# Kernel tuning notes

Measured on AMD Instinct MI355X. Metric: run time of the kernel, lower is better.

Reference implementation:

```python
import jax, jax.numpy as jnp
import numpy as np

B, T, E = 2, 2048, 2048
H, KV, D = 16, 4, 128
N_REP = H // KV
WINDOW = 512
BASE_THETA = 10000.0
MIN_VAL = -1e9


def _rope_cos_sin(seq_len, dim, dtype):
    inv_freq = 1.0 / (BASE_THETA ** (jnp.arange(0, dim, 2, dtype=jnp.float32) / dim))
    ang = jnp.arange(seq_len, dtype=jnp.float32)[:, None] * inv_freq[None, :]  # [T, D/2]
    return jnp.cos(ang).astype(dtype), jnp.sin(ang).astype(dtype)


def _apply_rope(x, cos, sin):
    # x: [B, T, h, D]; rotate-half convention
    x1, x2 = jnp.split(x, 2, axis=-1)
    c = cos[None, :, None, :]
    s = sin[None, :, None, :]
    return jnp.concatenate([x1 * c - x2 * s, x2 * c + x1 * s], axis=-1)


def setup_inputs() -> dict:
    key = jax.random.key(0)
    k1, k2, k3, k4, k5 = jax.random.split(key, 5)
    std = 0.02 / np.sqrt(2 * 24)
    return {
        "x": jax.random.normal(k1, (B, T, E), dtype=jnp.float32),
        "Wq": jax.random.normal(k2, (H * D, E), dtype=jnp.float32) * std,
        "Wk": jax.random.normal(k3, (KV * D, E), dtype=jnp.float32) * std,
        "Wv": jax.random.normal(k4, (KV * D, E), dtype=jnp.float32) * std,
        "Wo": jax.random.normal(k5, (E, E), dtype=jnp.float32) * std,
    }


def reference(x, Wq, Wk, Wv, Wo):
    b, t, e = x.shape
    scale = 1.0 / jnp.sqrt(jnp.float32(D))

    q = (x @ Wq.T).reshape(b, t, H, D)
    k = (x @ Wk.T).reshape(b, t, KV, D)
    v = (x @ Wv.T).reshape(b, t, KV, D)

    cos, sin = _rope_cos_sin(t, D, x.dtype)
    q = _apply_rope(q, cos, sin)
    k = _apply_rope(k, cos, sin)

    # GQA: repeat kv heads to match query heads
    k = jnp.repeat(k, N_REP, axis=2)  # [B, T, H, D]
    v = jnp.repeat(v, N_REP, axis=2)

    scores = jnp.einsum("bqhd,bkhd->bhqk", q, k) * scale  # [B, H, T, T]

    # sliding-window causal additive mask (offset=0)
    rows = jnp.arange(t)[:, None]
    cols = jnp.arange(t)[None, :]
    valid = (cols <= rows) & ((rows - cols) < WINDOW)
    mask = jnp.where(valid, 0.0, MIN_VAL).astype(x.dtype)  # [T, T]
    scores = scores + mask[None, None, :, :]

    attn = jax.nn.softmax(scores, axis=-1)
    out = jnp.einsum("bhqk,bkhd->bqhd", attn, v).reshape(b, t, H * D)
    return out @ Wo.T
```

## Files before the change

### kernel.cpp

```cpp
#include <hip/hip_runtime.h>
#include <hip/hip_bf16.h>
#include <cstdint>

#define TSEQ 2048
#define NB   2
#define NH   16
#define NKV  4
#define HD   128
#define EMB  2048
#define WIN  512

typedef unsigned short u16;
typedef __attribute__((ext_vector_type(8))) short s16x8;
typedef __attribute__((ext_vector_type(4))) float f32x4;
typedef __attribute__((ext_vector_type(16))) float f32x16;
typedef __attribute__((ext_vector_type(4))) unsigned short u16x4;
typedef __attribute__((ext_vector_type(8))) unsigned short u16x8;

__device__ __forceinline__ u16 f2bf(float x) {
    unsigned u = __builtin_bit_cast(unsigned, x);
    u += 0x7fffu + ((u >> 16) & 1u);
    return (u16)(u >> 16);
}
__device__ __forceinline__ float bf2f(u16 u) {
    return __builtin_bit_cast(float, ((unsigned)u) << 16);
}
__device__ __forceinline__ float ex2(float x) {
    return __builtin_amdgcn_exp2f(x);
}

__device__ __forceinline__ void gld_lds16(const void* g, void* l) {
    __builtin_amdgcn_global_load_lds(
        (__attribute__((address_space(1))) void*)(void*)(g),
        (__attribute__((address_space(3))) void*)(l),
        16, 0, 0);
}

__device__ __forceinline__ f32x4 mfma16(s16x8 a, s16x8 b, f32x4 c) {
    return __builtin_amdgcn_mfma_f32_16x16x32_bf16(a, b, c, 0, 0, 0);
}
__device__ __forceinline__ f32x16 mfma32(s16x8 a, s16x8 b, f32x16 c) {
    return __builtin_amdgcn_mfma_f32_32x32x16_bf16(a, b, c, 0, 0, 0);
}

template <int CTRL>
__device__ __forceinline__ float dpp_movf(float x) {
    return __builtin_bit_cast(float,
        __builtin_amdgcn_update_dpp(0, __builtin_bit_cast(int, x), CTRL, 0xF, 0xF, true));
}
__device__ __forceinline__ float dpp_max16(float x) {
    x = fmaxf(x, dpp_movf<0xB1>(x));
    x = fmaxf(x, dpp_movf<0x4E>(x));
    x = fmaxf(x, dpp_movf<0x128>(x));
    x = fmaxf(x, dpp_movf<0x124>(x));
    return x;
}
__device__ __forceinline__ float dpp_sum16(float x) {
    x += dpp_movf<0xB1>(x);
    x += dpp_movf<0x4E>(x);
    x += dpp_movf<0x128>(x);
    x += dpp_movf<0x124>(x);
    return x;
}

__global__ void cast_all(const float* __restrict__ x,  const float* __restrict__ wq,
                         const float* __restrict__ wk, const float* __restrict__ wv,
                         const float* __restrict__ wo,
                         u16* __restrict__ xb, u16* __restrict__ wqb,
                         u16* __restrict__ wkvb, u16* __restrict__ wob,
                         float* __restrict__ tab) {
    if (blockIdx.x >= 18432) {
        int i = (blockIdx.x - 18432) * 256 + threadIdx.x;
        int t = i >> 6, d = i & 63;
        float inv = __expf(-(float)d * (9.210340371976184f / 64.0f));
        float s, c;
        sincosf((float)t * inv, &s, &c);
        tab[i] = c;
        tab[131072 + i] = s;
        return;
    }
    long i = ((long)blockIdx.x * 256 + threadIdx.x) * 4;
    const float* s; u16* d; long off;
    if (i < 8388608L)        { s = x;  d = xb;             off = i; }
    else if (i < 12582912L)  { s = wq; d = wqb;            off = i - 8388608L; }
    else if (i < 13631488L)  { s = wk; d = wkvb;           off = i - 12582912L; }
    else if (i < 14680064L)  { s = wv; d = wkvb + 1048576; off = i - 13631488L; }
    else                     { s = wo; d = wob;            off = i - 14680064L; }
    float4 v = *(const float4*)(s + off);
    u16x4 o;
    o[0] = f2bf(v.x); o[1] = f2bf(v.y); o[2] = f2bf(v.z); o[3] = f2bf(v.w);
    *(u16x4*)(d + off) = o;
}

template <int MODE>
__global__ __launch_bounds__(256) void gemm_bt(const u16* __restrict__ A, const u16* __restrict__ B,
                                               void* __restrict__ Cp, u16* __restrict__ vtp,
                                               u16* __restrict__ kp,
                                               int M, int N, int K) {
    __shared__ __align__(16) u16 smem[16384];
    u16* As = smem;
    u16* Bs = smem + 8192;
    const int tid  = threadIdx.x;
    const int lane = tid & 63;
    const int w    = tid >> 6;
    const int l31  = lane & 31;
    const int half = lane >> 5;
    const int wr   = w >> 1, wc = w & 1;

    const int srow   = w * 8 + (lane >> 3);
    const int schunk = lane & 7;
    const u16* agp[4];
    const u16* bgp[4];
#pragma unroll
    for (int s = 0; s < 4; s++) {
        const int row = s * 32 + srow;
        const int sig = ((row >> 1) ^ (row >> 2)) & 7;
        agp[s] = A + (size_t)(blockIdx.y * 128 + row) * K + (schunk ^ sig) * 8;
        bgp[s] = B + (size_t)(blockIdx.x * 128 + row) * K + (schunk ^ sig) * 8;
    }

    int sigA[2], sigB[2];
#pragma unroll
    for (int i = 0; i < 2; i++) {
        const int ra = wr * 64 + i * 32 + l31;
        sigA[i] = ((ra >> 1) ^ (ra >> 2)) & 7;
        const int rb = wc * 64 + i * 32 + l31;
        sigB[i] = ((rb >> 1) ^ (rb >> 2)) & 7;
    }

    f32x16 acc[2][2];
#pragma unroll
    for (int i = 0; i < 2; i++)
#pragma unroll
        for (int j = 0; j < 2; j++)
#pragma unroll
            for (int r = 0; r < 16; r++)
                acc[i][j][r] = 0.f;

    for (int k0 = 0; k0 < K; k0 += 64) {
#pragma unroll
        for (int s = 0; s < 4; s++) {
            gld_lds16(agp[s], (char*)As + (s * 32 + w * 8) * 128);
            agp[s] += 64;
        }
#pragma unroll
        for (int s = 0; s < 4; s++) {
            gld_lds16(bgp[s], (char*)Bs + (s * 32 + w * 8) * 128);
            bgp[s] += 64;
        }
        __syncthreads();
        s16x8 af[2][4], bf[2][4];
#pragma unroll
        for (int i = 0; i < 2; i++)
#pragma unroll
            for (int ks = 0; ks < 4; ks++)
                af[i][ks] = *(const s16x8*)((char*)As + (wr * 64 + i * 32 + l31) * 128 +
                                            ((half + ks * 2) ^ sigA[i]) * 16);
#pragma unroll
        for (int j = 0; j < 2; j++)
#pragma unroll
            for (int ks = 0; ks < 4; ks++)
                bf[j][ks] = *(const s16x8*)((char*)Bs + (wc * 64 + j * 32 + l31) * 128 +
                                            ((half + ks * 2) ^ sigB[j]) * 16);
#pragma unroll
        for (int ks = 0; ks < 4; ks++)
#pragma unroll
            for (int i = 0; i < 2; i++)
#pragma unroll
                for (int j = 0; j < 2; j++)
                    acc[i][j] = mfma32(af[i][ks], bf[j][ks], acc[i][j]);
        __syncthreads();
    }

    const int row0 = blockIdx.y * 128 + wr * 64;
    const int col0 = blockIdx.x * 128 + wc * 64 + l31;

    if (MODE == 0) {
#pragma unroll
        for (int i = 0; i < 2; i++)
#pragma unroll
            for (int j = 0; j < 2; j++)
#pragma unroll
                for (int r = 0; r < 16; r++) {
                    const int crow = row0 + i * 32 + (r & 3) + 8 * (r >> 2) + 4 * half;
                    ((float*)Cp)[(size_t)crow * N + col0 + j * 32] = acc[i][j][r];
                }
    } else {
        if (blockIdx.x < 16) {
#pragma unroll
            for (int i = 0; i < 2; i++)
#pragma unroll
                for (int j = 0; j < 2; j++)
#pragma unroll
                    for (int r = 0; r < 16; r++) {
                        const int crow = row0 + i * 32 + (r & 3) + 8 * (r >> 2) + 4 * half;
                        ((u16*)Cp)[(size_t)crow * 2048 + col0 + j * 32] = f2bf(acc[i][j][r]);
                    }
        } else if (blockIdx.x < 20) {
            const int kcol0 = col0 - 2048;
#pragma unroll
            for (int i = 0; i < 2; i++)
#pragma unroll
                for (int j = 0; j < 2; j++)
#pragma unroll
                    for (int r = 0; r < 16; r++) {
                        const int crow = row0 + i * 32 + (r & 3) + 8 * (r >> 2) + 4 * half;
                        kp[(size_t)crow * 512 + kcol0 + j * 32] = f2bf(acc[i][j][r]);
                    }
        } else {
            const int kvi = blockIdx.x - 20;
            const int bb  = (blockIdx.y * 128) >> 11;
            const int tl0 = (blockIdx.y * 128) & (TSEQ - 1);
            u16* tr = smem;
#pragma unroll
            for (int p = 0; p < 2; p++) {
                __syncthreads();
                if (wc == p) {
#pragma unroll
                    for (int i = 0; i < 2; i++)
#pragma unroll
                        for (int j = 0; j < 2; j++)
#pragma unroll
                            for (int r = 0; r < 16; r++) {
                                const int tl = wr * 64 + i * 32 + (r & 3) + 8 * (r >> 2) + 4 * half;
                                tr[(j * 32 + l31) * 136 + tl] = f2bf(acc[i][j][r]);
                            }
                }
                __syncthreads();
#pragma unroll
                for (int s = 0; s < 4; s++) {
                    int slot = s * 256 + tid;
                    int dr = slot >> 4;
                    int tc = slot & 15;
                    u16x8 val = *(const u16x8*)(tr + dr * 136 + tc * 8);
                    *(u16x8*)(vtp + ((size_t)((bb * NKV + kvi) * HD + p * 64 + dr)) * TSEQ +
                              tl0 + tc * 8) = val;
                }
            }
        }
    }
}

__global__ void rope_k(u16* __restrict__ buf, const float* __restrict__ tab) {
    int i = blockIdx.x * 256 + threadIdx.x;
    int d   = i & 63;
    int hh  = (i >> 6) & 3;
    int row = i >> 8;
    int t   = row & (TSEQ - 1);
    size_t base = (size_t)row * 512 + hh * HD + d;
    float x1 = bf2f(buf[base]);
    float x2 = bf2f(buf[base + 64]);
    float c = tab[t * 64 + d];
    float s = tab[131072 + t * 64 + d];
    buf[base]      = f2bf(x1 * c - x2 * s);
    buf[base + 64] = f2bf(x2 * c + x1 * s);
}

__global__ __launch_bounds__(256, 3) void attn_kernel(const u16* __restrict__ qb, const u16* __restrict__ kb,
                                                      const u16* __restrict__ vt, const float* __restrict__ tab,
                                                      u16* __restrict__ ao) {
    __shared__ __align__(16) char smem[40960];
    u16* ks = (u16*)smem;
    u16* vs = (u16*)(smem + 16384);
    u16* Pl = (u16*)(smem + 32768);

    const int tid  = threadIdx.x;
    const int w    = tid >> 6;
    const int lane = tid & 63;
    const int l15  = lane & 15;
    const int quad = lane >> 4;
    const int id   = blockIdx.x;
    const int kv   = id & 3;
    const int b    = (id >> 2) & 1;
    const int q0   = (id >> 3) * 16;
    const int h    = kv * 4 + w;
    u16* Pw = Pl + w * 1024;
    const float scale2 = 0.1275174089593282f;

    const u16* kbase = kb + (size_t)b * TSEQ * 512 + kv * HD;
    const u16* vbase = vt + (size_t)(b * NKV + kv) * HD * TSEQ;

    s16x8 aq[4];
    {
        const u16* qrow = qb + (size_t)(b * TSEQ + q0 + l15) * EMB + h * HD + quad * 8;
        const float* ct = tab + (size_t)(q0 + l15) * 64 + quad * 8;
        float qf[4][8], cs[2][8], sn[2][8];
        *(float4*)(&cs[0][0]) = *(const float4*)(ct);
        *(float4*)(&cs[0][4]) = *(const float4*)(ct + 4);
        *(float4*)(&cs[1][0]) = *(const float4*)(ct + 32);
        *(float4*)(&cs[1][4]) = *(const float4*)(ct + 36);
        *(float4*)(&sn[0][0]) = *(const float4*)(ct + 131072);
        *(float4*)(&sn[0][4]) = *(const float4*)(ct + 131076);
        *(float4*)(&sn[1][0]) = *(const float4*)(ct + 131104);
        *(float4*)(&sn[1][4]) = *(const float4*)(ct + 131108);
#pragma unroll
        for (int c = 0; c < 4; c++)
#pragma unroll
            for (int e = 0; e < 8; e++)
                qf[c][e] = bf2f(qrow[c * 32 + e]);
#pragma unroll
        for (int c = 0; c < 2; c++)
#pragma unroll
            for (int e = 0; e < 8; e++) {
                float x1 = qf[c][e], x2 = qf[c + 2][e];
                qf[c][e]     = x1 * cs[c][e] - x2 * sn[c][e];
                qf[c + 2][e] = x2 * cs[c][e] + x1 * sn[c][e];
            }
#pragma unroll
        for (int c = 0; c < 4; c++)
#pragma unroll
            for (int e = 0; e < 8; e++)
                aq[c][e] = (short)f2bf(qf[c][e]);
    }

    f32x4 o[8];
#pragma unroll
    for (int n = 0; n < 8; n++) o[n] = f32x4{0.f, 0.f, 0.f, 0.f};
    float mrow[4] = {-1e30f, -1e30f, -1e30f, -1e30f};
    float lrow[4] = {0.f, 0.f, 0.f, 0.f};

    int kb0 = q0 - (WIN - 1);
    if (kb0 < 0) kb0 = 0;
    kb0 &= ~63;

    for (int kbi = kb0; kbi <= q0 + 15; kbi += 64) {
#pragma unroll
        for (int s = 0; s < 4; s++) {
            int slot = s * 256 + tid;
            int i    = slot >> 4;
            int lc   = (slot & 15) ^ (i & 7);
            gld_lds16(kbase + (size_t)(kbi + i) * 512 + lc * 8, (char*)ks + slot * 16);
        }
#pragma unroll
        for (int s = 0; s < 4; s++) {
            int slot = s * 256 + tid;
            int d    = slot >> 3;
            int lc   = (slot & 7) ^ (d & 7);
            gld_lds16(vbase + (size_t)d * TSEQ + kbi + lc * 8, (char*)vs + slot * 16);
        }
        __syncthreads();

        f32x4 sv[4];
#pragma unroll
        for (int kt = 0; kt < 4; kt++) sv[kt] = f32x4{0.f, 0.f, 0.f, 0.f};
#pragma unroll
        for (int c = 0; c < 4; c++) {
            s16x8 bk[4];
#pragma unroll
            for (int kt = 0; kt < 4; kt++) {
                int sc = (c * 4 + quad) ^ (l15 & 7);
                bk[kt] = *(const s16x8*)(ks + (kt * 16 + l15) * 128 + sc * 8);
            }
#pragma unroll
            for (int kt = 0; kt < 4; kt++)
                sv[kt] = mfma16(aq[c], bk[kt], sv[kt]);
        }

        const bool full = (kbi >= q0 - 496) && (kbi + 63 <= q0);
        float alpha[4], p[4][4];
#pragma unroll
        for (int r = 0; r < 4; r++) {
            const int row = q0 + quad * 4 + r;
            float v[4];
            if (full) {
#pragma unroll
                for (int kt = 0; kt < 4; kt++) v[kt] = sv[kt][r] * scale2;
            } else {
#pragma unroll
                for (int kt = 0; kt < 4; kt++) {
                    int cidx = kbi + kt * 16 + l15;
                    v[kt] = (cidx <= row && row - cidx < WIN) ? sv[kt][r] * scale2 : -1e30f;
                }
            }
            float mx = fmaxf(fmaxf(v[0], v[1]), fmaxf(v[2], v[3]));
            mx = dpp_max16(mx);
            float mnew = fmaxf(mrow[r], mx);
            alpha[r] = ex2(mrow[r] - mnew);
            float e0 = ex2(v[0] - mnew);
            float e1 = ex2(v[1] - mnew);
            float e2 = ex2(v[2] - mnew);
            float e3 = ex2(v[3] - mnew);
            float rs = (e0 + e1) + (e2 + e3);
            rs = dpp_sum16(rs);
            lrow[r] = lrow[r] * alpha[r] + rs;
            mrow[r] = mnew;
            p[0][r] = e0; p[1][r] = e1; p[2][r] = e2; p[3][r] = e3;
        }
#pragma unroll
        for (int n = 0; n < 8; n++) {
            o[n][0] *= alpha[0]; o[n][1] *= alpha[1];
            o[n][2] *= alpha[2]; o[n][3] *= alpha[3];
        }

#pragma unroll
        for (int r = 0; r < 4; r++)
#pragma unroll
            for (int kt = 0; kt < 4; kt++)
                Pw[(kt >> 1) * 512 + (quad * 4 + r) * 32 + (kt & 1) * 16 + l15] = f2bf(p[kt][r]);
        asm volatile("s_waitcnt lgkmcnt(0)" ::: "memory");
        s16x8 ap0 = *(const s16x8*)(Pw + l15 * 32 + quad * 8);
        s16x8 ap1 = *(const s16x8*)(Pw + 512 + l15 * 32 + quad * 8);

#pragma unroll
        for (int n = 0; n < 8; n++) {
            int sc = quad ^ (l15 & 7);
            s16x8 bv = *(const s16x8*)(vs + (n * 16 + l15) * 64 + sc * 8);
            o[n] = mfma16(ap0, bv, o[n]);
        }
#pragma unroll
        for (int n = 0; n < 8; n++) {
            int sc = (4 + quad) ^ (l15 & 7);
            s16x8 bv = *(const s16x8*)(vs + (n * 16 + l15) * 64 + sc * 8);
            o[n] = mfma16(ap1, bv, o[n]);
        }
        __syncthreads();
    }

    float linv[4];
#pragma unroll
    for (int r = 0; r < 4; r++) linv[r] = 1.0f / lrow[r];
    u16* Ow = (u16*)(smem + w * 4352);
#pragma unroll
    for (int n = 0; n < 8; n++)
#pragma unroll
        for (int r = 0; r < 4; r++)
            Ow[(quad * 4 + r) * 136 + n * 16 + l15] = f2bf(o[n][r] * linv[r]);
    asm volatile("s_waitcnt lgkmcnt(0)" ::: "memory");
#pragma unroll
    for (int s = 0; s < 4; s++) {
        int row = s * 4 + quad;
        u16x8 val = *(const u16x8*)(Ow + row * 136 + l15 * 8);
        *(u16x8*)(ao + (size_t)(b * TSEQ + q0 + row) * EMB + h * HD + l15 * 8) = val;
    }
}

extern "C" void kernel_launch(void* const* d_in, const int* in_sizes, int n_in,
                              void* d_out, int out_size, void* d_ws, size_t ws_size,
                              hipStream_t stream) {
    const float* x  = (const float*)d_in[0];
    const float* Wq = (const float*)d_in[1];
    const float* Wk = (const float*)d_in[2];
    const float* Wv = (const float*)d_in[3];
    const float* Wo = (const float*)d_in[4];
    float* out = (float*)d_out;

    u16* ws   = (u16*)d_ws;
    u16* xb   = ws;
    u16* wqb  = ws + 8388608L;
    u16* wkvb = ws + 12582912L;
    u16* wob  = ws + 14680064L;
    u16* qb   = ws + 18874368L;
    u16* kbuf = ws + 27262976L;
    u16* vt   = ws + 29360128L;
    float* tab = (float*)(ws + 31457280L);
    u16* ao   = xb;

    cast_all<<<18944, 256, 0, stream>>>(x, Wq, Wk, Wv, Wo, xb, wqb, wkvb, wob, tab);

    gemm_bt<3><<<dim3(24, 32), 256, 0, stream>>>(xb, wqb, qb, vt, kbuf, 4096, 3072, 2048);

    rope_k<<<4096, 256, 0, stream>>>(kbuf, tab);

    attn_kernel<<<1024, 256, 0, stream>>>(qb, kbuf, vt, tab, ao);

    gemm_bt<0><<<dim3(16, 32), 256, 0, stream>>>(ao, wob, out, nullptr, nullptr, 4096, 2048, 2048);
}
```

Measured before the change: 255.1 us.

## Rewrite GEMMs as 8-wave double-buffered kernels with larger tiles and interleaved loads

Replaces the 256-thread 128x128 GEMM with a 512-thread kernel using 256x256 tiles for the QKV projection and 256x128 tiles for the output projection. LDS is double-buffered, and global-to-LDS loads for tile t+2 are issued between MFMA phases, with partial vmcnt waits, barriers and s_setprio to overlap memory with compute. The aim is more operand reuse and hidden load latency in both projection GEMMs. The cost is fewer blocks (192 and 256) on a 256-CU part, plus higher register and LDS pressure.

```diff
diff --git a/kernel.cpp b/kernel.cpp
--- a/kernel.cpp
+++ b/kernel.cpp
@@ -92,149 +92,259 @@
     *(u16x4*)(d + off) = o;
 }
 
+#define RDFRAG(base, offb, sg, ks) \
+    (*(const s16x8*)((base) + (offb) + ((((half) + 2 * (ks)) ^ (sg)) << 4)))
+
 template <int MODE>
-__global__ __launch_bounds__(256) void gemm_bt(const u16* __restrict__ A, const u16* __restrict__ B,
-                                               void* __restrict__ Cp, u16* __restrict__ vtp,
-                                               u16* __restrict__ kp,
-                                               int M, int N, int K) {
-    __shared__ __align__(16) u16 smem[16384];
-    u16* As = smem;
-    u16* Bs = smem + 8192;
+__global__ __launch_bounds__(512) void gemm8(const u16* __restrict__ A, const u16* __restrict__ B,
+                                             void* __restrict__ Cp, u16* __restrict__ vtp,
+                                             u16* __restrict__ kp) {
+    constexpr int BN     = (MODE == 3) ? 256 : 128;
+    constexpr int NBB    = BN / 64;
+    constexpr int MT     = (MODE == 3) ? 4 : 2;
+    constexpr int WM     = MT * 32;
+    constexpr int K      = 2048;
+    constexpr int NTK    = K / 64;
+    constexpr int ABYTES = 32768;
+    constexpr int BBYTES = BN * 128;
+    constexpr int BUFB   = ABYTES + BBYTES;
+
+    __shared__ __align__(16) char smem[2 * BUFB];
+
     const int tid  = threadIdx.x;
     const int lane = tid & 63;
     const int w    = tid >> 6;
     const int l31  = lane & 31;
     const int half = lane >> 5;
-    const int wr   = w >> 1, wc = w & 1;
+    const int wr   = (MODE == 3) ? (w >> 2) : (w >> 1);
+    const int wc   = (MODE == 3) ? (w & 3) : (w & 1);
+    const int bx   = blockIdx.x, by = blockIdx.y;
 
     const int srow   = w * 8 + (lane >> 3);
     const int schunk = lane & 7;
+    const int sdoff  = w * 8 * 128;
+
     const u16* agp[4];
-    const u16* bgp[4];
+    const u16* bgp[NBB];
 #pragma unroll
     for (int s = 0; s < 4; s++) {
-        const int row = s * 32 + srow;
-        const int sig = ((row >> 1) ^ (row >> 2)) & 7;
-        agp[s] = A + (size_t)(blockIdx.y * 128 + row) * K + (schunk ^ sig) * 8;
-        bgp[s] = B + (size_t)(blockIdx.x * 128 + row) * K + (schunk ^ sig) * 8;
-    }
-
-    int sigA[2], sigB[2];
-#pragma unroll
-    for (int i = 0; i < 2; i++) {
-        const int ra = wr * 64 + i * 32 + l31;
-        sigA[i] = ((ra >> 1) ^ (ra >> 2)) & 7;
-        const int rb = wc * 64 + i * 32 + l31;
-        sigB[i] = ((rb >> 1) ^ (rb >> 2)) & 7;
-    }
-
-    f32x16 acc[2][2];
-#pragma unroll
-    for (int i = 0; i < 2; i++)
-#pragma unroll
-        for (int j = 0; j < 2; j++)
+        const int row = s * 64 + srow;
+        const int sg  = ((row >> 1) ^ (row >> 2)) & 7;
+        agp[s] = A + (size_t)(by * 256 + row) * K + ((schunk ^ sg) << 3);
+    }
+#pragma unroll
+    for (int s = 0; s < NBB; s++) {
+        const int row = s * 64 + srow;
+        const int sg  = ((row >> 1) ^ (row >> 2)) & 7;
+        bgp[s] = B + (size_t)(bx * BN + row) * K + ((schunk ^ sg) << 3);
+    }
+
+    int aoffb[MT], asg[MT];
+#pragma unroll
+    for (int mi = 0; mi < MT; mi++) {
+        const int r = wr * WM + mi * 32 + l31;
+        aoffb[mi] = r * 128;
+        asg[mi]   = ((r >> 1) ^ (r >> 2)) & 7;
+    }
+    int boffb[2], bsg[2];
+#pragma unroll
+    for (int nj = 0; nj < 2; nj++) {
+        const int r = wc * 64 + nj * 32 + l31;
+        boffb[nj] = r * 128;
+        bsg[nj]   = ((r >> 1) ^ (r >> 2)) & 7;
+    }
+
+    f32x16 acc[MT][2];
+#pragma unroll
+    for (int mi = 0; mi < MT; mi++)
+#pragma unroll
+        for (int nj = 0; nj < 2; nj++)
 #pragma unroll
             for (int r = 0; r < 16; r++)
-                acc[i][j][r] = 0.f;
-
-    for (int k0 = 0; k0 < K; k0 += 64) {
-#pragma unroll
-        for (int s = 0; s < 4; s++) {
-            gld_lds16(agp[s], (char*)As + (s * 32 + w * 8) * 128);
-            agp[s] += 64;
-        }
-#pragma unroll
-        for (int s = 0; s < 4; s++) {
-            gld_lds16(bgp[s], (char*)Bs + (s * 32 + w * 8) * 128);
+                acc[mi][nj][r] = 0.f;
+
+    auto stage_a02 = [&](char* base) {
+        gld_lds16(agp[0], base + sdoff);          agp[0] += 64;
+        gld_lds16(agp[2], base + 16384 + sdoff);  agp[2] += 64;
+    };
+    auto stage_rest = [&](char* base) {
+        gld_lds16(agp[1], base + 8192 + sdoff);   agp[1] += 64;
+        gld_lds16(agp[3], base + 24576 + sdoff);  agp[3] += 64;
+#pragma unroll
+        for (int s = 0; s < NBB; s++) {
+            gld_lds16(bgp[s], base + ABYTES + s * 8192 + sdoff);
             bgp[s] += 64;
         }
-        __syncthreads();
-        s16x8 af[2][4], bf[2][4];
-#pragma unroll
-        for (int i = 0; i < 2; i++)
+    };
+
+    stage_a02(smem);        stage_rest(smem);
+    stage_a02(smem + BUFB); stage_rest(smem + BUFB);
+
+    for (int t = 0; t < NTK; ++t) {
+        char* buf = smem + (t & 1) * BUFB;
+        const char* Ab = buf;
+        const char* Bb = buf + ABYTES;
+        if (t < NTK - 1) {
+            if constexpr (MODE == 3) asm volatile("s_waitcnt vmcnt(8)" ::: "memory");
+            else                     asm volatile("s_waitcnt vmcnt(6)" ::: "memory");
+        } else {
+            asm volatile("s_waitcnt vmcnt(0)" ::: "memory");
+        }
+        __builtin_amdgcn_s_barrier();
+
+        if constexpr (MODE == 3) {
+            s16x8 aA[4], aB[4], bA[4], bB[4];
+#pragma unroll
+            for (int ks = 0; ks < 4; ks++) {
+                aA[ks] = RDFRAG(Ab, aoffb[0], asg[0], ks);
+                aB[ks] = RDFRAG(Ab, aoffb[1], asg[1], ks);
+                bA[ks] = RDFRAG(Bb, boffb[0], bsg[0], ks);
+            }
+            __builtin_amdgcn_s_barrier();
+            __builtin_amdgcn_s_setprio(1);
+#pragma unroll
+            for (int ks = 0; ks < 4; ks++) {
+                acc[0][0] = mfma32(aA[ks], bA[ks], acc[0][0]);
+                acc[1][0] = mfma32(aB[ks], bA[ks], acc[1][0]);
+            }
+            __builtin_amdgcn_s_setprio(0);
+            __builtin_amdgcn_s_barrier();
 #pragma unroll
             for (int ks = 0; ks < 4; ks++)
-                af[i][ks] = *(const s16x8*)((char*)As + (wr * 64 + i * 32 + l31) * 128 +
-                                            ((half + ks * 2) ^ sigA[i]) * 16);
-#pragma unroll
-        for (int j = 0; j < 2; j++)
+                bB[ks] = RDFRAG(Bb, boffb[1], bsg[1], ks);
+            __builtin_amdgcn_s_barrier();
+            __builtin_amdgcn_s_setprio(1);
+#pragma unroll
+            for (int ks = 0; ks < 4; ks++) {
+                acc[0][1] = mfma32(aA[ks], bB[ks], acc[0][1]);
+                acc[1][1] = mfma32(aB[ks], bB[ks], acc[1][1]);
+            }
+            __builtin_amdgcn_s_setprio(0);
+            __builtin_amdgcn_s_barrier();
+            asm volatile("" ::: "memory");
+            if (t + 2 < NTK) stage_a02(buf);
+#pragma unroll
+            for (int ks = 0; ks < 4; ks++) {
+                aA[ks] = RDFRAG(Ab, aoffb[2], asg[2], ks);
+                aB[ks] = RDFRAG(Ab, aoffb[3], asg[3], ks);
+            }
+            __builtin_amdgcn_s_barrier();
+            __builtin_amdgcn_s_setprio(1);
+#pragma unroll
+            for (int ks = 0; ks < 4; ks++) {
+                acc[2][1] = mfma32(aA[ks], bB[ks], acc[2][1]);
+                acc[3][1] = mfma32(aB[ks], bB[ks], acc[3][1]);
+            }
+            __builtin_amdgcn_s_setprio(0);
+            __builtin_amdgcn_s_barrier();
+            __builtin_amdgcn_s_setprio(1);
+#pragma unroll
+            for (int ks = 0; ks < 4; ks++) {
+                acc[2][0] = mfma32(aA[ks], bA[ks], acc[2][0]);
+                acc[3][0] = mfma32(aB[ks], bA[ks], acc[3][0]);
+            }
+            __builtin_amdgcn_s_setprio(0);
+            __builtin_amdgcn_s_barrier();
+            asm volatile("" ::: "memory");
+            if (t + 2 < NTK) stage_rest(buf);
+        } else {
+            s16x8 aA[4], aB[4], bA[4], bB[4];
+#pragma unroll
+            for (int ks = 0; ks < 4; ks++) {
+                aA[ks] = RDFRAG(Ab, aoffb[0], asg[0], ks);
+                bA[ks] = RDFRAG(Bb, boffb[0], bsg[0], ks);
+                bB[ks] = RDFRAG(Bb, boffb[1], bsg[1], ks);
+            }
+            __builtin_amdgcn_s_barrier();
+            __builtin_amdgcn_s_setprio(1);
+#pragma unroll
+            for (int ks = 0; ks < 4; ks++) {
+                acc[0][0] = mfma32(aA[ks], bA[ks], acc[0][0]);
+                acc[0][1] = mfma32(aA[ks], bB[ks], acc[0][1]);
+            }
+            __builtin_amdgcn_s_setprio(0);
+            __builtin_amdgcn_s_barrier();
 #pragma unroll
             for (int ks = 0; ks < 4; ks++)
-                bf[j][ks] = *(const s16x8*)((char*)Bs + (wc * 64 + j * 32 + l31) * 128 +
-                                            ((half + ks * 2) ^ sigB[j]) * 16);
-#pragma unroll
-        for (int ks = 0; ks < 4; ks++)
-#pragma unroll
-            for (int i = 0; i < 2; i++)
-#pragma unroll
-                for (int j = 0; j < 2; j++)
-                    acc[i][j] = mfma32(af[i][ks], bf[j][ks], acc[i][j]);
-        __syncthreads();
-    }
-
-    const int row0 = blockIdx.y * 128 + wr * 64;
-    const int col0 = blockIdx.x * 128 + wc * 64 + l31;
-
-    if (MODE == 0) {
-#pragma unroll
-        for (int i = 0; i < 2; i++)
-#pragma unroll
-            for (int j = 0; j < 2; j++)
+                aB[ks] = RDFRAG(Ab, aoffb[1], asg[1], ks);
+            __builtin_amdgcn_s_barrier();
+            __builtin_amdgcn_s_setprio(1);
+#pragma unroll
+            for (int ks = 0; ks < 4; ks++) {
+                acc[1][0] = mfma32(aB[ks], bA[ks], acc[1][0]);
+                acc[1][1] = mfma32(aB[ks], bB[ks], acc[1][1]);
+            }
+            __builtin_amdgcn_s_setprio(0);
+            __builtin_amdgcn_s_barrier();
+            asm volatile("" ::: "memory");
+            if (t + 2 < NTK) { stage_a02(buf); stage_rest(buf); }
+        }
+    }
+
+    const int row0 = by * 256 + wr * WM;
+    if constexpr (MODE == 0) {
+        const int col0 = bx * BN + wc * 64 + l31;
+#pragma unroll
+        for (int mi = 0; mi < MT; mi++)
+#pragma unroll
+            for (int nj = 0; nj < 2; nj++)
 #pragma unroll
                 for (int r = 0; r < 16; r++) {
-                    const int crow = row0 + i * 32 + (r & 3) + 8 * (r >> 2) + 4 * half;
-                    ((float*)Cp)[(size_t)crow * N + col0 + j * 32] = acc[i][j][r];
+                    const int crow = row0 + mi * 32 + (r & 3) + 8 * (r >> 2) + 4 * half;
+                    ((float*)Cp)[(size_t)crow * 2048 + col0 + nj * 32] = acc[mi][nj][r];
                 }
     } else {
-        if (blockIdx.x < 16) {
-#pragma unroll
-            for (int i = 0; i < 2; i++)
-#pragma unroll
-                for (int j = 0; j < 2; j++)
+        if (bx < 8) {
+            const int col0 = bx * 256 + wc * 64 + l31;
+#pragma unroll
+            for (int mi = 0; mi < MT; mi++)
+#pragma unroll
+                for (int nj = 0; nj < 2; nj++)
 #pragma unroll
                     for (int r = 0; r < 16; r++) {
-                        const int crow = row0 + i * 32 + (r & 3) + 8 * (r >> 2) + 4 * half;
-                        ((u16*)Cp)[(size_t)crow * 2048 + col0 + j * 32] = f2bf(acc[i][j][r]);
+                        const int crow = row0 + mi * 32 + (r & 3) + 8 * (r >> 2) + 4 * half;
+                        ((u16*)Cp)[(size_t)crow * 2048 + col0 + nj * 32] = f2bf(acc[mi][nj][r]);
                     }
-        } else if (blockIdx.x < 20) {
-            const int kcol0 = col0 - 2048;
-#pragma unroll
-            for (int i = 0; i < 2; i++)
-#pragma unroll
-                for (int j = 0; j < 2; j++)
+        } else if (bx < 10) {
+            const int kcol0 = (bx - 8) * 256 + wc * 64 + l31;
+#pragma unroll
+            for (int mi = 0; mi < MT; mi++)
+#pragma unroll
+                for (int nj = 0; nj < 2; nj++)
 #pragma unroll
                     for (int r = 0; r < 16; r++) {
-                        const int crow = row0 + i * 32 + (r & 3) + 8 * (r >> 2) + 4 * half;
-                        kp[(size_t)crow * 512 + kcol0 + j * 32] = f2bf(acc[i][j][r]);
+                        const int crow = row0 + mi * 32 + (r & 3) + 8 * (r >> 2) + 4 * half;
+                        kp[(size_t)crow * 512 + kcol0 + nj * 32] = f2bf(acc[mi][nj][r]);
                     }
         } else {
-            const int kvi = blockIdx.x - 20;
-            const int bb  = (blockIdx.y * 128) >> 11;
-            const int tl0 = (blockIdx.y * 128) & (TSEQ - 1);
-            u16* tr = smem;
+            const int bb = (by * 256) >> 11;
+            const int t0 = (by * 256) & (TSEQ - 1);
+            u16* tr = (u16*)smem;
 #pragma unroll
             for (int p = 0; p < 2; p++) {
                 __syncthreads();
-                if (wc == p) {
-#pragma unroll
-                    for (int i = 0; i < 2; i++)
-#pragma unroll
-                        for (int j = 0; j < 2; j++)
+                if ((wc >> 1) == p) {
+#pragma unroll
+                    for (int mi = 0; mi < MT; mi++)
+#pragma unroll
+                        for (int nj = 0; nj < 2; nj++)
 #pragma unroll
                             for (int r = 0; r < 16; r++) {
-                                const int tl = wr * 64 + i * 32 + (r & 3) + 8 * (r >> 2) + 4 * half;
-                                tr[(j * 32 + l31) * 136 + tl] = f2bf(acc[i][j][r]);
+                                const int tl = wr * 128 + mi * 32 + (r & 3) + 8 * (r >> 2) + 4 * half;
+                                const int cl = (wc & 1) * 64 + nj * 32 + l31;
+                                tr[cl * 264 + tl] = f2bf(acc[mi][nj][r]);
                             }
                 }
                 __syncthreads();
 #pragma unroll
-                for (int s = 0; s < 4; s++) {
-                    int slot = s * 256 + tid;
-                    int dr = slot >> 4;
-                    int tc = slot & 15;
-                    u16x8 val = *(const u16x8*)(tr + dr * 136 + tc * 8);
-                    *(u16x8*)(vtp + ((size_t)((bb * NKV + kvi) * HD + p * 64 + dr)) * TSEQ +
-                              tl0 + tc * 8) = val;
+                for (int s = 0; s < 8; s++) {
+                    const int slot = s * 512 + tid;
+                    const int dcol = slot >> 5;
+                    const int tseg = slot & 31;
+                    u16x8 val = *(const u16x8*)(tr + dcol * 264 + tseg * 8);
+                    const int vcol = (bx - 10) * 256 + p * 128 + dcol;
+                    *(u16x8*)(vtp + ((size_t)((bb * NKV + (vcol >> 7)) * HD + (vcol & 127))) * TSEQ +
+                              t0 + tseg * 8) = val;
                 }
             }
         }
@@ -457,11 +567,11 @@
 
     cast_all<<<18944, 256, 0, stream>>>(x, Wq, Wk, Wv, Wo, xb, wqb, wkvb, wob, tab);
 
-    gemm_bt<3><<<dim3(24, 32), 256, 0, stream>>>(xb, wqb, qb, vt, kbuf, 4096, 3072, 2048);
+    gemm8<3><<<dim3(12, 16), 512, 0, stream>>>(xb, wqb, qb, vt, kbuf);
 
     rope_k<<<4096, 256, 0, stream>>>(kbuf, tab);
 
     attn_kernel<<<1024, 256, 0, stream>>>(qb, kbuf, vt, tab, ao);
 
-    gemm_bt<0><<<dim3(16, 32), 256, 0, stream>>>(ao, wob, out, nullptr, nullptr, 4096, 2048, 2048);
-}
+    gemm8<0><<<dim3(16, 16), 512, 0, stream>>>(ao, wob, out, nullptr, nullptr);
+}
```

After: 262.2 us. 2.8% more time.

## Double-buffer K/V tiles in attention kernel to overlap loads with compute

Applied to the files above, without the earlier changes.

Attention kernel now keeps two LDS buffers for K and V tiles and issues the async global-to-LDS load for the next key block before computing on the current one. It waits with a partial vmcnt so only the current tile's loads must land. This aims to hide global memory latency behind the MFMA work. In exchange LDS grows to 72KB and the launch-bounds occupancy target drops from 3 to 2 blocks per CU, so there is less latency hiding from extra waves.

```diff
diff --git a/kernel.cpp b/kernel.cpp
--- a/kernel.cpp
+++ b/kernel.cpp
@@ -256,13 +256,13 @@
     buf[base + 64] = f2bf(x2 * c + x1 * s);
 }
 
-__global__ __launch_bounds__(256, 3) void attn_kernel(const u16* __restrict__ qb, const u16* __restrict__ kb,
+__global__ __launch_bounds__(256, 2) void attn_kernel(const u16* __restrict__ qb, const u16* __restrict__ kb,
                                                       const u16* __restrict__ vt, const float* __restrict__ tab,
                                                       u16* __restrict__ ao) {
-    __shared__ __align__(16) char smem[40960];
+    __shared__ __align__(16) char smem[73728];
     u16* ks = (u16*)smem;
-    u16* vs = (u16*)(smem + 16384);
-    u16* Pl = (u16*)(smem + 32768);
+    u16* vs = (u16*)(smem + 32768);
+    u16* Pl = (u16*)(smem + 65536);
 
     const int tid  = threadIdx.x;
     const int w    = tid >> 6;
@@ -322,23 +322,43 @@
     int kb0 = q0 - (WIN - 1);
     if (kb0 < 0) kb0 = 0;
     kb0 &= ~63;
-
-    for (int kbi = kb0; kbi <= q0 + 15; kbi += 64) {
+    const int nt = ((q0 + 15 - kb0) >> 6) + 1;
+
+    auto stage = [&](int kbi, int sel) {
+        char* ksb = (char*)ks + sel * 16384;
+        char* vsb = (char*)vs + sel * 16384;
 #pragma unroll
         for (int s = 0; s < 4; s++) {
             int slot = s * 256 + tid;
             int i    = slot >> 4;
             int lc   = (slot & 15) ^ (i & 7);
-            gld_lds16(kbase + (size_t)(kbi + i) * 512 + lc * 8, (char*)ks + slot * 16);
+            gld_lds16(kbase + (size_t)(kbi + i) * 512 + lc * 8, ksb + slot * 16);
         }
 #pragma unroll
         for (int s = 0; s < 4; s++) {
             int slot = s * 256 + tid;
             int d    = slot >> 3;
             int lc   = (slot & 7) ^ (d & 7);
-            gld_lds16(vbase + (size_t)d * TSEQ + kbi + lc * 8, (char*)vs + slot * 16);
-        }
-        __syncthreads();
+            gld_lds16(vbase + (size_t)d * TSEQ + kbi + lc * 8, vsb + slot * 16);
+        }
+    };
+
+    stage(kb0, 0);
+
+    for (int it = 0; it < nt; ++it) {
+        const int kbi = kb0 + it * 64;
+        const int cur = it & 1;
+        const u16* ksb = (const u16*)((const char*)ks + cur * 16384);
+        const u16* vsb = (const u16*)((const char*)vs + cur * 16384);
+
+        if (it + 1 < nt) {
+            stage(kbi + 64, cur ^ 1);
+            asm volatile("s_waitcnt vmcnt(8)" ::: "memory");
+        } else {
+            asm volatile("s_waitcnt vmcnt(0)" ::: "memory");
+        }
+        __builtin_amdgcn_s_barrier();
+        __builtin_amdgcn_sched_barrier(0);
 
         f32x4 sv[4];
 #pragma unroll
@@ -349,7 +369,7 @@
 #pragma unroll
             for (int kt = 0; kt < 4; kt++) {
                 int sc = (c * 4 + quad) ^ (l15 & 7);
-                bk[kt] = *(const s16x8*)(ks + (kt * 16 + l15) * 128 + sc * 8);
+                bk[kt] = *(const s16x8*)(ksb + (kt * 16 + l15) * 128 + sc * 8);
             }
 #pragma unroll
             for (int kt = 0; kt < 4; kt++)
@@ -404,16 +424,18 @@
 #pragma unroll
         for (int n = 0; n < 8; n++) {
             int sc = quad ^ (l15 & 7);
-            s16x8 bv = *(const s16x8*)(vs + (n * 16 + l15) * 64 + sc * 8);
+            s16x8 bv = *(const s16x8*)(vsb + (n * 16 + l15) * 64 + sc * 8);
             o[n] = mfma16(ap0, bv, o[n]);
         }
 #pragma unroll
         for (int n = 0; n < 8; n++) {
             int sc = (4 + quad) ^ (l15 & 7);
-            s16x8 bv = *(const s16x8*)(vs + (n * 16 + l15) * 64 + sc * 8);
+            s16x8 bv = *(const s16x8*)(vsb + (n * 16 + l15) * 64 + sc * 8);
             o[n] = mfma16(ap1, bv, o[n]);
         }
-        __syncthreads();
+        asm volatile("s_waitcnt lgkmcnt(0)" ::: "memory");
+        __builtin_amdgcn_sched_barrier(0);
+        __builtin_amdgcn_s_barrier();
     }
 
     float linv[4];
```

Result: slower. 266.5 us (+4.5%).

## Fuse K RoPE into QKV GEMM epilogue and raise attention occupancy

Applied to the files above, without the earlier changes.

Applies rotary embedding to K inside the QKV GEMM epilogue by staging the tile in shared memory, which removes the separate rope kernel launch and its global read-modify-write pass. Raises the attention kernel's launch-bounds occupancy hint from 3 to 4 waves per SIMD. Wraps the attention MFMA loops in s_setprio to favour matrix issue. The higher occupancy target may force register spills, and the staged epilogue adds an extra LDS round trip.

```diff
diff --git a/kernel.cpp b/kernel.cpp
--- a/kernel.cpp
+++ b/kernel.cpp
@@ -95,7 +95,7 @@
 template <int MODE>
 __global__ __launch_bounds__(256) void gemm_bt(const u16* __restrict__ A, const u16* __restrict__ B,
                                                void* __restrict__ Cp, u16* __restrict__ vtp,
-                                               u16* __restrict__ kp,
+                                               u16* __restrict__ kp, const float* __restrict__ tab,
                                                int M, int N, int K) {
     __shared__ __align__(16) u16 smem[16384];
     u16* As = smem;
@@ -197,16 +197,33 @@
                         ((u16*)Cp)[(size_t)crow * 2048 + col0 + j * 32] = f2bf(acc[i][j][r]);
                     }
         } else if (blockIdx.x < 20) {
-            const int kcol0 = col0 - 2048;
+            const int head = blockIdx.x - 16;
+            u16* kl = smem;
 #pragma unroll
             for (int i = 0; i < 2; i++)
 #pragma unroll
                 for (int j = 0; j < 2; j++)
 #pragma unroll
                     for (int r = 0; r < 16; r++) {
-                        const int crow = row0 + i * 32 + (r & 3) + 8 * (r >> 2) + 4 * half;
-                        kp[(size_t)crow * 512 + kcol0 + j * 32] = f2bf(acc[i][j][r]);
+                        const int tl = wr * 64 + i * 32 + (r & 3) + 8 * (r >> 2) + 4 * half;
+                        const int cl = wc * 64 + j * 32 + l31;
+                        kl[tl * 128 + cl] = f2bf(acc[i][j][r]);
                     }
+            __syncthreads();
+#pragma unroll
+            for (int s = 0; s < 32; s++) {
+                const int idx = s * 256 + tid;
+                const int row = idx >> 6;
+                const int d   = idx & 63;
+                const float x1 = bf2f(kl[row * 128 + d]);
+                const float x2 = bf2f(kl[row * 128 + d + 64]);
+                const int grow = blockIdx.y * 128 + row;
+                const int t    = grow & (TSEQ - 1);
+                const float c  = tab[t * 64 + d];
+                const float sn = tab[131072 + t * 64 + d];
+                kp[(size_t)grow * 512 + head * 128 + d]      = f2bf(x1 * c - x2 * sn);
+                kp[(size_t)grow * 512 + head * 128 + d + 64] = f2bf(x2 * c + x1 * sn);
+            }
         } else {
             const int kvi = blockIdx.x - 20;
             const int bb  = (blockIdx.y * 128) >> 11;
@@ -241,22 +258,7 @@
     }
 }
 
-__global__ void rope_k(u16* __restrict__ buf, const float* __restrict__ tab) {
-    int i = blockIdx.x * 256 + threadIdx.x;
-    int d   = i & 63;
-    int hh  = (i >> 6) & 3;
-    int row = i >> 8;
-    int t   = row & (TSEQ - 1);
-    size_t base = (size_t)row * 512 + hh * HD + d;
-    float x1 = bf2f(buf[base]);
-    float x2 = bf2f(buf[base + 64]);
-    float c = tab[t * 64 + d];
-    float s = tab[131072 + t * 64 + d];
-    buf[base]      = f2bf(x1 * c - x2 * s);
-    buf[base + 64] = f2bf(x2 * c + x1 * s);
-}
-
-__global__ __launch_bounds__(256, 3) void attn_kernel(const u16* __restrict__ qb, const u16* __restrict__ kb,
+__global__ __launch_bounds__(256, 4) void attn_kernel(const u16* __restrict__ qb, const u16* __restrict__ kb,
                                                       const u16* __restrict__ vt, const float* __restrict__ tab,
                                                       u16* __restrict__ ao) {
     __shared__ __align__(16) char smem[40960];
@@ -343,6 +345,7 @@
         f32x4 sv[4];
 #pragma unroll
         for (int kt = 0; kt < 4; kt++) sv[kt] = f32x4{0.f, 0.f, 0.f, 0.f};
+        __builtin_amdgcn_s_setprio(1);
 #pragma unroll
         for (int c = 0; c < 4; c++) {
             s16x8 bk[4];
@@ -355,6 +358,7 @@
             for (int kt = 0; kt < 4; kt++)
                 sv[kt] = mfma16(aq[c], bk[kt], sv[kt]);
         }
+        __builtin_amdgcn_s_setprio(0);
 
         const bool full = (kbi >= q0 - 496) && (kbi + 63 <= q0);
         float alpha[4], p[4][4];
@@ -401,6 +405,7 @@
         s16x8 ap0 = *(const s16x8*)(Pw + l15 * 32 + quad * 8);
         s16x8 ap1 = *(const s16x8*)(Pw + 512 + l15 * 32 + quad * 8);
 
+        __builtin_amdgcn_s_setprio(1);
 #pragma unroll
         for (int n = 0; n < 8; n++) {
             int sc = quad ^ (l15 & 7);
@@ -413,6 +418,7 @@
             s16x8 bv = *(const s16x8*)(vs + (n * 16 + l15) * 64 + sc * 8);
             o[n] = mfma16(ap1, bv, o[n]);
         }
+        __builtin_amdgcn_s_setprio(0);
         __syncthreads();
     }
 
@@ -457,11 +463,9 @@
 
     cast_all<<<18944, 256, 0, stream>>>(x, Wq, Wk, Wv, Wo, xb, wqb, wkvb, wob, tab);
 
-    gemm_bt<3><<<dim3(24, 32), 256, 0, stream>>>(xb, wqb, qb, vt, kbuf, 4096, 3072, 2048);
-
-    rope_k<<<4096, 256, 0, stream>>>(kbuf, tab);
+    gemm_bt<3><<<dim3(24, 32), 256, 0, stream>>>(xb, wqb, qb, vt, kbuf, tab, 4096, 3072, 2048);
 
     attn_kernel<<<1024, 256, 0, stream>>>(qb, kbuf, vt, tab, ao);
 
-    gemm_bt<0><<<dim3(16, 32), 256, 0, stream>>>(ao, wob, out, nullptr, nullptr, 4096, 2048, 2048);
-}
+    gemm_bt<0><<<dim3(16, 32), 256, 0, stream>>>(ao, wob, out, nullptr, nullptr, nullptr, 4096, 2048, 2048);
+}
```

New measurement: 249.7 us, median of 3. 2.1% less time.
